# Kernel optimization log

Hardware: AMD Instinct MI355X
Metric: run time of the kernel (lower is better)

Reference implementation:

```python
import jax, jax.numpy as jnp
import numpy as np

D_MODEL = 1024
N_LAYER = 4
D_INNER = 2048   # expand * d_model
D_STATE = 16
D_CONV = 4
DT_RANK = 64     # ceil(d_model / 16)
B, L = 2, 1024
EPS = 1e-5


def setup_inputs() -> dict:
    key = jax.random.key(0)
    ks = jax.random.split(key, 10)
    nl = N_LAYER
    def nrm(k, shape, s=0.02):
        return jax.random.normal(k, shape, jnp.float32) * s
    A_log = jnp.broadcast_to(jnp.log(jnp.arange(1, D_STATE + 1, dtype=jnp.float32)),
                             (nl, D_INNER, D_STATE)) + jnp.zeros((nl, D_INNER, D_STATE), jnp.float32)
    return {
        "hidden_states": jax.random.normal(ks[0], (B, L, D_MODEL), jnp.float32),
        "in_proj_w": nrm(ks[1], (nl, 2 * D_INNER, D_MODEL)),
        "conv_w": nrm(ks[2], (nl, D_INNER, D_CONV), 0.1),
        "conv_b": nrm(ks[3], (nl, D_INNER), 0.02),
        "x_proj_w": nrm(ks[4], (nl, DT_RANK + 2 * D_STATE, D_INNER)),
        "dt_proj_w": nrm(ks[5], (nl, D_INNER, DT_RANK), DT_RANK ** -0.5),
        "dt_proj_b": jnp.log(jnp.expm1(jax.random.uniform(ks[6], (nl, D_INNER), jnp.float32, 1e-3, 0.1))),
        "A_log": A_log,
        "D": jnp.ones((nl, D_INNER), jnp.float32),
        "out_proj_w": nrm(ks[7], (nl, D_MODEL, D_INNER)),
        "norm_w": jnp.ones((nl, D_MODEL), jnp.float32),
        "norm_b": jnp.zeros((nl, D_MODEL), jnp.float32),
        "normf_w": jnp.ones((D_MODEL,), jnp.float32),
        "normf_b": jnp.zeros((D_MODEL,), jnp.float32),
    }


def _layernorm(x, w, b):
    mu = x.mean(-1, keepdims=True)
    var = ((x - mu) ** 2).mean(-1, keepdims=True)
    return (x - mu) * jax.lax.rsqrt(var + EPS) * w + b


def _mamba(h, iw, cw, cb, xw, dw, db, Alog, Dp, ow):
    Bn, Ln, _ = h.shape
    xz = jnp.einsum('bld,ed->ble', h, iw)          # [B,L,2*d_inner]
    x, z = jnp.split(xz, 2, axis=-1)
    # depthwise causal conv1d over time, kernel size D_CONV
    xp = jnp.pad(x, ((0, 0), (D_CONV - 1, 0), (0, 0)))
    xc = sum(xp[:, k:k + Ln, :] * cw[:, k] for k in range(D_CONV)) + cb
    x = jax.nn.silu(xc)
    dbl = jnp.einsum('bld,ed->ble', x, xw)         # [B,L,dt_rank+2*d_state]
    dt = dbl[..., :DT_RANK]
    Bm = dbl[..., DT_RANK:DT_RANK + D_STATE]
    Cm = dbl[..., DT_RANK + D_STATE:]
    dt = jax.nn.softplus(jnp.einsum('blr,dr->bld', dt, dw) + db)  # [B,L,d_inner]
    A = -jnp.exp(Alog)                              # [d_inner,d_state]

    def step(hc, inp):
        dt_t, B_t, C_t, x_t = inp                   # [B,d],[B,s],[B,s],[B,d]
        dA = jnp.exp(dt_t[:, :, None] * A)
        hc = hc * dA + (dt_t * x_t)[:, :, None] * B_t[:, None, :]
        y_t = jnp.einsum('bds,bs->bd', hc, C_t)
        return hc, y_t

    h0 = jnp.zeros((Bn, D_INNER, D_STATE), x.dtype)
    xs = (dt.transpose(1, 0, 2), Bm.transpose(1, 0, 2),
          Cm.transpose(1, 0, 2), x.transpose(1, 0, 2))
    _, ys = jax.lax.scan(step, h0, xs)              # ys: [L,B,d_inner]
    y = ys.transpose(1, 0, 2) + x * Dp
    y = y * jax.nn.silu(z)
    return jnp.einsum('bld,ed->ble', y, ow)


def reference(hidden_states, in_proj_w, conv_w, conv_b, x_proj_w, dt_proj_w,
              dt_proj_b, A_log, D, out_proj_w, norm_w, norm_b, normf_w, normf_b):
    hs = hidden_states
    residual = None
    for i in range(N_LAYER):
        residual = hs if residual is None else hs + residual
        hs = _layernorm(residual, norm_w[i], norm_b[i])
        hs = _mamba(hs, in_proj_w[i], conv_w[i], conv_b[i], x_proj_w[i],
                    dt_proj_w[i], dt_proj_b[i], A_log[i], D[i], out_proj_w[i])
    residual = hs + residual
    return _layernorm(residual, normf_w, normf_b)
```

## Files before the change

### kernel.cpp

```cpp
#include <hip/hip_runtime.h>
#include <math.h>

#define D_MODEL 1024
#define D_INNER 2048
#define D_STATE 16
#define D_CONV  4
#define DT_RANK 64
#define NB      2
#define LSEQ    1024
#define NROWS   (NB * LSEQ)
#define LN_EPS  1e-5f
#define N_LAYER 4
#define NCHUNK  32
#define TCH     (LSEQ / NCHUNK)

__device__ inline unsigned bfbits(float f) {
    unsigned u = __float_as_uint(f);
    return (u + 0x7fffu + ((u >> 16) & 1u)) >> 16;
}

__device__ inline float wave_sum(float s) {
    #pragma unroll
    for (int m = 1; m < 64; m <<= 1) s += __shfl_xor(s, m, 64);
    return s;
}

__global__ __launch_bounds__(256)
void add_ln_kernel(const float* __restrict__ add, float* __restrict__ residual,
                   const float* __restrict__ w, const float* __restrict__ b,
                   void* __restrict__ out, int first, int bf16out)
{
    int row = blockIdx.x;
    int tid = threadIdx.x;
    size_t base = (size_t)row * D_MODEL + tid * 4;

    float4 v = *(const float4*)(add + base);
    if (!first) {
        float4 r = *(const float4*)(residual + base);
        v.x += r.x; v.y += r.y; v.z += r.z; v.w += r.w;
    }
    *(float4*)(residual + base) = v;

    __shared__ float red[8];
    float s = v.x + v.y + v.z + v.w;
    s = wave_sum(s);
    if ((tid & 63) == 0) red[tid >> 6] = s;
    __syncthreads();
    float mu = (red[0] + red[1] + red[2] + red[3]) * (1.0f / D_MODEL);

    float dx = v.x - mu, dy = v.y - mu, dz = v.z - mu, dw2 = v.w - mu;
    float s2 = dx*dx + dy*dy + dz*dz + dw2*dw2;
    s2 = wave_sum(s2);
    if ((tid & 63) == 0) red[4 + (tid >> 6)] = s2;
    __syncthreads();
    float var = (red[4] + red[5] + red[6] + red[7]) * (1.0f / D_MODEL);
    float rs = rsqrtf(var + LN_EPS);

    float4 wv = *(const float4*)(w + tid * 4);
    float4 bv = *(const float4*)(b + tid * 4);
    float4 o;
    o.x = dx  * rs * wv.x + bv.x;
    o.y = dy  * rs * wv.y + bv.y;
    o.z = dz  * rs * wv.z + bv.z;
    o.w = dw2 * rs * wv.w + bv.w;
    if (bf16out) {
        ushort4 ov;
        ov.x = (unsigned short)bfbits(o.x);
        ov.y = (unsigned short)bfbits(o.y);
        ov.z = (unsigned short)bfbits(o.z);
        ov.w = (unsigned short)bfbits(o.w);
        *(ushort4*)((unsigned short*)out + base) = ov;
    } else {
        *(float4*)((float*)out + base) = o;
    }
}

__global__ __launch_bounds__(256)
void f32_to_bf16_kernel(const float* __restrict__ src, unsigned short* __restrict__ dst)
{
    int i = blockIdx.x * 256 + threadIdx.x;
    float4 v = *(const float4*)(src + (size_t)i * 4);
    ushort4 o;
    o.x = (unsigned short)bfbits(v.x);
    o.y = (unsigned short)bfbits(v.y);
    o.z = (unsigned short)bfbits(v.z);
    o.w = (unsigned short)bfbits(v.w);
    *(ushort4*)(dst + (size_t)i * 4) = o;
}

#define TILE 64
#define KT   16

__global__ __launch_bounds__(256)
void gemm_nt(const float* __restrict__ A, const float* __restrict__ B,
             float* __restrict__ C, int M, int N, int K,
             int lda, int ldb, int ldc,
             const float* __restrict__ bias, int mode)
{
    __shared__ float As[KT][TILE + 4];
    __shared__ float Bs[KT][TILE + 4];

    int tid = threadIdx.x;
    int tx = tid & 15, ty = tid >> 4;
    int m0 = blockIdx.y * TILE;
    int n0 = blockIdx.x * TILE;

    int lr = tid >> 2;
    int lk = (tid & 3) * 4;

    float acc[4][4] = {};

    for (int k0 = 0; k0 < K; k0 += KT) {
        {
            int m = m0 + lr;
            float4 v = *(const float4*)(A + (size_t)m * lda + k0 + lk);
            As[lk + 0][lr] = v.x; As[lk + 1][lr] = v.y;
            As[lk + 2][lr] = v.z; As[lk + 3][lr] = v.w;
        }
        {
            int n = n0 + lr;
            float4 v = make_float4(0.f, 0.f, 0.f, 0.f);
            if (n < N) v = *(const float4*)(B + (size_t)n * ldb + k0 + lk);
            Bs[lk + 0][lr] = v.x; Bs[lk + 1][lr] = v.y;
            Bs[lk + 2][lr] = v.z; Bs[lk + 3][lr] = v.w;
        }
        __syncthreads();
        #pragma unroll
        for (int kk = 0; kk < KT; ++kk) {
            float4 a4 = *(const float4*)&As[kk][ty * 4];
            float4 b4 = *(const float4*)&Bs[kk][tx * 4];
            float av[4] = {a4.x, a4.y, a4.z, a4.w};
            float bv[4] = {b4.x, b4.y, b4.z, b4.w};
            #pragma unroll
            for (int i = 0; i < 4; ++i)
                #pragma unroll
                for (int j = 0; j < 4; ++j)
                    acc[i][j] += av[i] * bv[j];
        }
        __syncthreads();
    }

    #pragma unroll
    for (int i = 0; i < 4; ++i) {
        int m = m0 + ty * 4 + i;
        #pragma unroll
        for (int j = 0; j < 4; ++j) {
            int n = n0 + tx * 4 + j;
            if (n >= N) continue;
            float v = acc[i][j];
            if (mode == 1) {
                v += bias[n];
                v = (v > 20.f) ? v : log1pf(__expf(v));
            }
            C[(size_t)m * ldc + n] = v;
        }
    }
}

__global__ __launch_bounds__(256)
void gemm_nt_splitk(const float* __restrict__ A, const float* __restrict__ B,
                    float* __restrict__ C, int M, int N, int K,
                    int lda, int ldb, int ldc, int kslice)
{
    __shared__ float As[KT][TILE + 4];
    __shared__ float Bs[KT][TILE + 4];

    int tid = threadIdx.x;
    int tx = tid & 15, ty = tid >> 4;
    int m0 = blockIdx.y * TILE;
    int n0 = blockIdx.x * TILE;
    int kb = blockIdx.z * kslice;

    int lr = tid >> 2;
    int lk = (tid & 3) * 4;

    float acc[4][4] = {};

    for (int k0 = kb; k0 < kb + kslice; k0 += KT) {
        {
            int m = m0 + lr;
            float4 v = *(const float4*)(A + (size_t)m * lda + k0 + lk);
            As[lk + 0][lr] = v.x; As[lk + 1][lr] = v.y;
            As[lk + 2][lr] = v.z; As[lk + 3][lr] = v.w;
        }
        {
            int n = n0 + lr;
            float4 v = make_float4(0.f, 0.f, 0.f, 0.f);
            if (n < N) v = *(const float4*)(B + (size_t)n * ldb + k0 + lk);
            Bs[lk + 0][lr] = v.x; Bs[lk + 1][lr] = v.y;
            Bs[lk + 2][lr] = v.z; Bs[lk + 3][lr] = v.w;
        }
        __syncthreads();
        #pragma unroll
        for (int kk = 0; kk < KT; ++kk) {
            float4 a4 = *(const float4*)&As[kk][ty * 4];
            float4 b4 = *(const float4*)&Bs[kk][tx * 4];
            float av[4] = {a4.x, a4.y, a4.z, a4.w};
            float bv[4] = {b4.x, b4.y, b4.z, b4.w};
            #pragma unroll
            for (int i = 0; i < 4; ++i)
                #pragma unroll
                for (int j = 0; j < 4; ++j)
                    acc[i][j] += av[i] * bv[j];
        }
        __syncthreads();
    }

    #pragma unroll
    for (int i = 0; i < 4; ++i) {
        int m = m0 + ty * 4 + i;
        #pragma unroll
        for (int j = 0; j < 4; ++j) {
            int n = n0 + tx * 4 + j;
            if (n < N) atomicAdd(&C[(size_t)m * ldc + n], acc[i][j]);
        }
    }
}

using bf16x8 = __attribute__((ext_vector_type(8))) short;
using f32x4  = __attribute__((ext_vector_type(4))) float;

#define BBM 128
#define BBN 128
#define BBK 64
#define LDS_S (BBK + 8)

__global__ __launch_bounds__(256)
void gemm_bf16_nt(const unsigned short* __restrict__ A, const unsigned short* __restrict__ Bw,
                  float* __restrict__ C, int M, int N, int K)
{
    __shared__ unsigned short As[BBM * LDS_S];
    __shared__ unsigned short Bs[BBN * LDS_S];

    int tid = threadIdx.x;
    int m0 = blockIdx.y * BBM, n0 = blockIdx.x * BBN;
    int lane = tid & 63, w = tid >> 6;
    int wm = (w >> 1) * 64, wn = (w & 1) * 64;
    int lm = lane & 15, q = lane >> 4;

    int lr = tid >> 3;
    int lc = (tid & 7) * 8;

    f32x4 acc[4][4] = {};

    for (int k0 = 0; k0 < K; k0 += BBK) {
        #pragma unroll
        for (int r = 0; r < 4; ++r) {
            int row = lr + r * 32;
            uint4 av = *(const uint4*)(A + (size_t)(m0 + row) * K + k0 + lc);
            *(uint4*)&As[row * LDS_S + lc] = av;
        }
        #pragma unroll
        for (int r = 0; r < 4; ++r) {
            int row = lr + r * 32;
            uint4 pv = *(const uint4*)(Bw + (size_t)(n0 + row) * K + k0 + lc);
            *(uint4*)&Bs[row * LDS_S + lc] = pv;
        }
        __syncthreads();
        #pragma unroll
        for (int kk = 0; kk < BBK; kk += 32) {
            bf16x8 af[4], bf[4];
            #pragma unroll
            for (int i = 0; i < 4; ++i)
                af[i] = *(const bf16x8*)&As[(wm + i * 16 + lm) * LDS_S + kk + q * 8];
            #pragma unroll
            for (int j = 0; j < 4; ++j)
                bf[j] = *(const bf16x8*)&Bs[(wn + j * 16 + lm) * LDS_S + kk + q * 8];
            #pragma unroll
            for (int i = 0; i < 4; ++i)
                #pragma unroll
                for (int j = 0; j < 4; ++j)
                    acc[i][j] = __builtin_amdgcn_mfma_f32_16x16x32_bf16(
                        af[i], bf[j], acc[i][j], 0, 0, 0);
        }
        __syncthreads();
    }

    #pragma unroll
    for (int i = 0; i < 4; ++i)
        #pragma unroll
        for (int j = 0; j < 4; ++j)
            #pragma unroll
            for (int r = 0; r < 4; ++r) {
                int row = m0 + wm + i * 16 + q * 4 + r;
                int col = n0 + wn + j * 16 + lm;
                C[(size_t)row * N + col] = acc[i][j][r];
            }
}

__global__ __launch_bounds__(256)
void conv_silu_kernel(const float* __restrict__ xz, const float* __restrict__ cw,
                      const float* __restrict__ cb, float* __restrict__ xc)
{
    int idx = blockIdx.x * 256 + threadIdx.x;
    int d  = idx & (D_INNER - 1);
    int t  = (idx >> 11) & (LSEQ - 1);
    int bb = idx >> 21;

    const float* xcol = xz + (size_t)bb * LSEQ * 2 * D_INNER + d;
    float acc = cb[d];
    #pragma unroll
    for (int k = 0; k < D_CONV; ++k) {
        int tt = t + k - (D_CONV - 1);
        if (tt >= 0) acc += xcol[(size_t)tt * 2 * D_INNER] * cw[d * D_CONV + k];
    }
    acc = acc / (1.f + __expf(-acc));
    xc[idx] = acc;
}

#define UNPK4(dst, off, v) { dst[(off)+0]=(v).x; dst[(off)+1]=(v).y; \
                             dst[(off)+2]=(v).z; dst[(off)+3]=(v).w; }

__global__ __launch_bounds__(256)
void scan_pass1(const float* __restrict__ dtb, const float* __restrict__ xc,
                const float* __restrict__ dbl, const float* __restrict__ Alog,
                float* __restrict__ aPbuf, float* __restrict__ bAbuf)
{
    int tid  = threadIdx.x;
    int half = tid & 1;
    int blk  = blockIdx.x;
    int dg   = blk & 15;
    int c    = (blk >> 4) & (NCHUNK - 1);
    int bb   = blk >> 9;
    int d    = dg * 128 + (tid >> 1);

    float A[8];
    {
        const float* pA = Alog + (size_t)d * D_STATE + half * 8;
        float4 v0 = *(const float4*)pA;
        float4 v1 = *(const float4*)(pA + 4);
        A[0] = -__expf(v0.x); A[1] = -__expf(v0.y);
        A[2] = -__expf(v0.z); A[3] = -__expf(v0.w);
        A[4] = -__expf(v1.x); A[5] = -__expf(v1.y);
        A[6] = -__expf(v1.z); A[7] = -__expf(v1.w);
    }

    size_t rowbase = (size_t)bb * LSEQ + (size_t)c * TCH;
    const float* pdt = dtb + rowbase * D_INNER + d;
    const float* pxc = xc  + rowbase * D_INNER + d;
    const float* pbc = dbl + rowbase * 96 + DT_RANK + half * 8;

    float aP[8] = {1.f,1.f,1.f,1.f,1.f,1.f,1.f,1.f};
    float bA[8] = {0.f,0.f,0.f,0.f,0.f,0.f,0.f,0.f};

    float  dtE = pdt[0], xvE = pxc[0];
    float4 BE0 = *(const float4*)pbc;
    float4 BE1 = *(const float4*)(pbc + 4);
    float  dtO = pdt[D_INNER], xvO = pxc[D_INNER];
    float4 BO0 = *(const float4*)(pbc + 96);
    float4 BO1 = *(const float4*)(pbc + 96 + 4);

    for (int t = 0; t < TCH; t += 2) {
        int t2 = (t + 2 < TCH) ? t + 2 : TCH - 1;
        int t3 = (t + 3 < TCH) ? t + 3 : TCH - 1;
        float  dtEn = pdt[(size_t)t2 * D_INNER], xvEn = pxc[(size_t)t2 * D_INNER];
        float4 BE0n = *(const float4*)(pbc + (size_t)t2 * 96);
        float4 BE1n = *(const float4*)(pbc + (size_t)t2 * 96 + 4);
        float  dtOn = pdt[(size_t)t3 * D_INNER], xvOn = pxc[(size_t)t3 * D_INNER];
        float4 BO0n = *(const float4*)(pbc + (size_t)t3 * 96);
        float4 BO1n = *(const float4*)(pbc + (size_t)t3 * 96 + 4);

        {
            float B[8];
            UNPK4(B, 0, BE0) UNPK4(B, 4, BE1)
            float dtx = dtE * xvE;
            #pragma unroll
            for (int s = 0; s < 8; ++s) {
                float a = __expf(dtE * A[s]);
                aP[s] *= a;
                bA[s] = bA[s] * a + dtx * B[s];
            }
        }
        {
            float B[8];
            UNPK4(B, 0, BO0) UNPK4(B, 4, BO1)
            float dtx = dtO * xvO;
            #pragma unroll
            for (int s = 0; s < 8; ++s) {
                float a = __expf(dtO * A[s]);
                aP[s] *= a;
                bA[s] = bA[s] * a + dtx * B[s];
            }
        }
        dtE = dtEn; xvE = xvEn; BE0 = BE0n; BE1 = BE1n;
        dtO = dtOn; xvO = xvOn; BO0 = BO0n; BO1 = BO1n;
    }

    float* pa = aPbuf + ((size_t)(bb * NCHUNK + c) * D_INNER + d) * D_STATE + half * 8;
    float* pb = bAbuf + ((size_t)(bb * NCHUNK + c) * D_INNER + d) * D_STATE + half * 8;
    *(float4*)(pa + 0) = make_float4(aP[0], aP[1], aP[2], aP[3]);
    *(float4*)(pa + 4) = make_float4(aP[4], aP[5], aP[6], aP[7]);
    *(float4*)(pb + 0) = make_float4(bA[0], bA[1], bA[2], bA[3]);
    *(float4*)(pb + 4) = make_float4(bA[4], bA[5], bA[6], bA[7]);
}

__global__ __launch_bounds__(256)
void scan_pass2(const float* __restrict__ dtb, const float* __restrict__ xc,
                const float* __restrict__ dbl, const float* __restrict__ xz,
                const float* __restrict__ Alog, const float* __restrict__ Dp,
                const float* __restrict__ aPbuf, const float* __restrict__ bAbuf,
                unsigned short* __restrict__ y)
{
    int tid  = threadIdx.x;
    int half = tid & 1;
    int blk  = blockIdx.x;
    int dg   = blk & 15;
    int c    = (blk >> 4) & (NCHUNK - 1);
    int bb   = blk >> 9;
    int d    = dg * 128 + (tid >> 1);

    float A[8];
    {
        const float* pA = Alog + (size_t)d * D_STATE + half * 8;
        float4 v0 = *(const float4*)pA;
        float4 v1 = *(const float4*)(pA + 4);
        A[0] = -__expf(v0.x); A[1] = -__expf(v0.y);
        A[2] = -__expf(v0.z); A[3] = -__expf(v0.w);
        A[4] = -__expf(v1.x); A[5] = -__expf(v1.y);
        A[6] = -__expf(v1.z); A[7] = -__expf(v1.w);
    }
    float Dd = Dp[d];

    float h[8] = {0.f,0.f,0.f,0.f,0.f,0.f,0.f,0.f};

    for (int cc = 0; cc < c; ++cc) {
        const float* pa = aPbuf + ((size_t)(bb * NCHUNK + cc) * D_INNER + d) * D_STATE + half * 8;
        const float* pb = bAbuf + ((size_t)(bb * NCHUNK + cc) * D_INNER + d) * D_STATE + half * 8;
        float4 a0 = *(const float4*)(pa + 0), a1 = *(const float4*)(pa + 4);
        float4 b0 = *(const float4*)(pb + 0), b1 = *(const float4*)(pb + 4);
        float av[8], bv[8];
        UNPK4(av, 0, a0) UNPK4(av, 4, a1)
        UNPK4(bv, 0, b0) UNPK4(bv, 4, b1)
        #pragma unroll
        for (int s = 0; s < 8; ++s) h[s] = h[s] * av[s] + bv[s];
    }

    size_t rowbase = (size_t)bb * LSEQ + (size_t)c * TCH;
    const float* pdt = dtb + rowbase * D_INNER + d;
    const float* pxc = xc  + rowbase * D_INNER + d;
    const float* pz  = xz  + rowbase * 2 * D_INNER + D_INNER + d;
    const float* pbc = dbl + rowbase * 96 + DT_RANK + half * 8;
    unsigned short* py = y + rowbase * D_INNER + d;

    float  dtE = pdt[0], xvE = pxc[0], zvE = pz[0];
    float4 BE0 = *(const float4*)pbc;
    float4 BE1 = *(const float4*)(pbc + 4);
    float4 CE0 = *(const float4*)(pbc + 16);
    float4 CE1 = *(const float4*)(pbc + 20);
    float  dtO = pdt[D_INNER], xvO = pxc[D_INNER], zvO = pz[2 * D_INNER];
    float4 BO0 = *(const float4*)(pbc + 96);
    float4 BO1 = *(const float4*)(pbc + 96 + 4);
    float4 CO0 = *(const float4*)(pbc + 96 + 16);
    float4 CO1 = *(const float4*)(pbc + 96 + 20);

    for (int t = 0; t < TCH; t += 2) {
        int t2 = (t + 2 < TCH) ? t + 2 : TCH - 1;
        int t3 = (t + 3 < TCH) ? t + 3 : TCH - 1;
        float  dtEn = pdt[(size_t)t2 * D_INNER], xvEn = pxc[(size_t)t2 * D_INNER];
        float  zvEn = pz[(size_t)t2 * 2 * D_INNER];
        float4 BE0n = *(const float4*)(pbc + (size_t)t2 * 96);
        float4 BE1n = *(const float4*)(pbc + (size_t)t2 * 96 + 4);
        float4 CE0n = *(const float4*)(pbc + (size_t)t2 * 96 + 16);
        float4 CE1n = *(const float4*)(pbc + (size_t)t2 * 96 + 20);
        float  dtOn = pdt[(size_t)t3 * D_INNER], xvOn = pxc[(size_t)t3 * D_INNER];
        float  zvOn = pz[(size_t)t3 * 2 * D_INNER];
        float4 BO0n = *(const float4*)(pbc + (size_t)t3 * 96);
        float4 BO1n = *(const float4*)(pbc + (size_t)t3 * 96 + 4);
        float4 CO0n = *(const float4*)(pbc + (size_t)t3 * 96 + 16);
        float4 CO1n = *(const float4*)(pbc + (size_t)t3 * 96 + 20);

        {
            float B[8], C[8];
            UNPK4(B, 0, BE0) UNPK4(B, 4, BE1)
            UNPK4(C, 0, CE0) UNPK4(C, 4, CE1)
            float dtx = dtE * xvE;
            float p = 0.f;
            #pragma unroll
            for (int s = 0; s < 8; ++s) {
                float a = __expf(dtE * A[s]);
                h[s] = h[s] * a + dtx * B[s];
                p += h[s] * C[s];
            }
            p += __shfl_xor(p, 1, 2);
            if (half == 0) {
                float sz = zvE / (1.f + __expf(-zvE));
                py[(size_t)t * D_INNER] = (unsigned short)bfbits((p + xvE * Dd) * sz);
            }
        }
        {
            float B[8], C[8];
            UNPK4(B, 0, BO0) UNPK4(B, 4, BO1)
            UNPK4(C, 0, CO0) UNPK4(C, 4, CO1)
            float dtx = dtO * xvO;
            float p = 0.f;
            #pragma unroll
            for (int s = 0; s < 8; ++s) {
                float a = __expf(dtO * A[s]);
                h[s] = h[s] * a + dtx * B[s];
                p += h[s] * C[s];
            }
            p += __shfl_xor(p, 1, 2);
            if (half == 0) {
                float sz = zvO / (1.f + __expf(-zvO));
                py[(size_t)(t + 1) * D_INNER] = (unsigned short)bfbits((p + xvO * Dd) * sz);
            }
        }
        dtE = dtEn; xvE = xvEn; zvE = zvEn;
        BE0 = BE0n; BE1 = BE1n; CE0 = CE0n; CE1 = CE1n;
        dtO = dtOn; xvO = xvOn; zvO = zvOn;
        BO0 = BO0n; BO1 = BO1n; CO0 = CO0n; CO1 = CO1n;
    }
}

extern "C" void kernel_launch(void* const* d_in, const int* in_sizes, int n_in,
                              void* d_out, int out_size, void* d_ws, size_t ws_size,
                              hipStream_t stream)
{
    const float* h_in  = (const float*)d_in[0];
    const float* iw    = (const float*)d_in[1];
    const float* cw    = (const float*)d_in[2];
    const float* cb    = (const float*)d_in[3];
    const float* xw    = (const float*)d_in[4];
    const float* dw    = (const float*)d_in[5];
    const float* db    = (const float*)d_in[6];
    const float* Alog  = (const float*)d_in[7];
    const float* Dp    = (const float*)d_in[8];
    const float* ow    = (const float*)d_in[9];
    const float* nw    = (const float*)d_in[10];
    const float* nb    = (const float*)d_in[11];
    const float* nfw   = (const float*)d_in[12];
    const float* nfb   = (const float*)d_in[13];

    float* ws = (float*)d_ws;
    float* residual = ws;
    float* hs       = residual + 2097152;
    float* xz       = hs + 2097152;
    float* xc       = xz + 8388608;
    float* dtb      = xc + 4194304;
    float* dbl      = dtb + 4194304;
    float* y        = dbl + 196608;

    float* aPbuf = hs;
    float* bAbuf = y + 2097152;

    unsigned short* wbuf_in  = (unsigned short*)y;
    unsigned short* hs_bf16  = (unsigned short*)(y + 2097152);
    unsigned short* y_bf16   = (unsigned short*)y;
    unsigned short* wbuf_out = (unsigned short*)dtb;

    const float* cur_add = h_in;
    for (int i = 0; i < N_LAYER; ++i) {
        add_ln_kernel<<<NROWS, 256, 0, stream>>>(cur_add, residual,
                                                 nw + i * D_MODEL, nb + i * D_MODEL,
                                                 hs_bf16, i == 0, 1);
        f32_to_bf16_kernel<<<(2 * D_INNER * D_MODEL) / 1024, 256, 0, stream>>>(
            iw + (size_t)i * 2 * D_INNER * D_MODEL, wbuf_in);
        gemm_bf16_nt<<<dim3(2 * D_INNER / BBN, NROWS / BBM), 256, 0, stream>>>(
            hs_bf16, wbuf_in, xz, NROWS, 2 * D_INNER, D_MODEL);
        conv_silu_kernel<<<NB * LSEQ * D_INNER / 256, 256, 0, stream>>>(
            xz, cw + (size_t)i * D_INNER * D_CONV, cb + i * D_INNER, xc);
        hipMemsetAsync(dbl, 0, 196608 * sizeof(float), stream);
        gemm_nt_splitk<<<dim3(2, NROWS / TILE, 8), 256, 0, stream>>>(
            xc, xw + (size_t)i * 96 * D_INNER, dbl,
            NROWS, 96, D_INNER, D_INNER, D_INNER, 96, D_INNER / 8);
        gemm_nt<<<dim3(D_INNER / TILE, NROWS / TILE), 256, 0, stream>>>(
            dbl, dw + (size_t)i * D_INNER * DT_RANK, dtb,
            NROWS, D_INNER, DT_RANK, 96, DT_RANK, D_INNER, db + i * D_INNER, 1);
        scan_pass1<<<NB * NCHUNK * (D_INNER / 128), 256, 0, stream>>>(
            dtb, xc, dbl, Alog + (size_t)i * D_INNER * D_STATE, aPbuf, bAbuf);
        scan_pass2<<<NB * NCHUNK * (D_INNER / 128), 256, 0, stream>>>(
            dtb, xc, dbl, xz, Alog + (size_t)i * D_INNER * D_STATE, Dp + i * D_INNER,
            aPbuf, bAbuf, y_bf16);
        f32_to_bf16_kernel<<<(D_MODEL * D_INNER) / 1024, 256, 0, stream>>>(
            ow + (size_t)i * D_MODEL * D_INNER, wbuf_out);
        gemm_bf16_nt<<<dim3(D_MODEL / BBN, NROWS / BBM), 256, 0, stream>>>(
            y_bf16, wbuf_out, hs, NROWS, D_MODEL, D_INNER);
        cur_add = hs;
    }
    add_ln_kernel<<<NROWS, 256, 0, stream>>>(hs, residual, nfw, nfb, d_out, 0, 0);
}
```

Baseline: 1.050 ms.

## Run x_proj and dt_proj GEMMs on MFMA using split bf16 hi/lo operands

Replaces the FP32 SIMT tiled GEMMs for x_proj (split-K with atomics) and dt_proj (with fused softplus) by MFMA kernels. Each operand is split into a bf16 high part and a bf16 low residual, and three MFMA products (hi*hi, hi*lo, lo*hi) approximate FP32 accuracy. The conv kernel now also emits the hi/lo copies of its output, and extra small kernels convert the weights and the dt-rank slice. This trades extra conversion passes and memory traffic for matrix-core throughput on two GEMMs that were running on scalar ALUs.

```diff
diff --git a/kernel.cpp b/kernel.cpp
--- a/kernel.cpp
+++ b/kernel.cpp
@@ -88,133 +88,37 @@
     *(ushort4*)(dst + (size_t)i * 4) = o;
 }
 
-#define TILE 64
-#define KT   16
-
-__global__ __launch_bounds__(256)
-void gemm_nt(const float* __restrict__ A, const float* __restrict__ B,
-             float* __restrict__ C, int M, int N, int K,
-             int lda, int ldb, int ldc,
-             const float* __restrict__ bias, int mode)
-{
-    __shared__ float As[KT][TILE + 4];
-    __shared__ float Bs[KT][TILE + 4];
-
-    int tid = threadIdx.x;
-    int tx = tid & 15, ty = tid >> 4;
-    int m0 = blockIdx.y * TILE;
-    int n0 = blockIdx.x * TILE;
-
-    int lr = tid >> 2;
-    int lk = (tid & 3) * 4;
-
-    float acc[4][4] = {};
-
-    for (int k0 = 0; k0 < K; k0 += KT) {
-        {
-            int m = m0 + lr;
-            float4 v = *(const float4*)(A + (size_t)m * lda + k0 + lk);
-            As[lk + 0][lr] = v.x; As[lk + 1][lr] = v.y;
-            As[lk + 2][lr] = v.z; As[lk + 3][lr] = v.w;
-        }
-        {
-            int n = n0 + lr;
-            float4 v = make_float4(0.f, 0.f, 0.f, 0.f);
-            if (n < N) v = *(const float4*)(B + (size_t)n * ldb + k0 + lk);
-            Bs[lk + 0][lr] = v.x; Bs[lk + 1][lr] = v.y;
-            Bs[lk + 2][lr] = v.z; Bs[lk + 3][lr] = v.w;
-        }
-        __syncthreads();
-        #pragma unroll
-        for (int kk = 0; kk < KT; ++kk) {
-            float4 a4 = *(const float4*)&As[kk][ty * 4];
-            float4 b4 = *(const float4*)&Bs[kk][tx * 4];
-            float av[4] = {a4.x, a4.y, a4.z, a4.w};
-            float bv[4] = {b4.x, b4.y, b4.z, b4.w};
-            #pragma unroll
-            for (int i = 0; i < 4; ++i)
-                #pragma unroll
-                for (int j = 0; j < 4; ++j)
-                    acc[i][j] += av[i] * bv[j];
-        }
-        __syncthreads();
-    }
-
-    #pragma unroll
-    for (int i = 0; i < 4; ++i) {
-        int m = m0 + ty * 4 + i;
-        #pragma unroll
-        for (int j = 0; j < 4; ++j) {
-            int n = n0 + tx * 4 + j;
-            if (n >= N) continue;
-            float v = acc[i][j];
-            if (mode == 1) {
-                v += bias[n];
-                v = (v > 20.f) ? v : log1pf(__expf(v));
-            }
-            C[(size_t)m * ldc + n] = v;
-        }
-    }
-}
-
-__global__ __launch_bounds__(256)
-void gemm_nt_splitk(const float* __restrict__ A, const float* __restrict__ B,
-                    float* __restrict__ C, int M, int N, int K,
-                    int lda, int ldb, int ldc, int kslice)
-{
-    __shared__ float As[KT][TILE + 4];
-    __shared__ float Bs[KT][TILE + 4];
-
-    int tid = threadIdx.x;
-    int tx = tid & 15, ty = tid >> 4;
-    int m0 = blockIdx.y * TILE;
-    int n0 = blockIdx.x * TILE;
-    int kb = blockIdx.z * kslice;
-
-    int lr = tid >> 2;
-    int lk = (tid & 3) * 4;
-
-    float acc[4][4] = {};
-
-    for (int k0 = kb; k0 < kb + kslice; k0 += KT) {
-        {
-            int m = m0 + lr;
-            float4 v = *(const float4*)(A + (size_t)m * lda + k0 + lk);
-            As[lk + 0][lr] = v.x; As[lk + 1][lr] = v.y;
-            As[lk + 2][lr] = v.z; As[lk + 3][lr] = v.w;
-        }
-        {
-            int n = n0 + lr;
-            float4 v = make_float4(0.f, 0.f, 0.f, 0.f);
-            if (n < N) v = *(const float4*)(B + (size_t)n * ldb + k0 + lk);
-            Bs[lk + 0][lr] = v.x; Bs[lk + 1][lr] = v.y;
-            Bs[lk + 2][lr] = v.z; Bs[lk + 3][lr] = v.w;
-        }
-        __syncthreads();
-        #pragma unroll
-        for (int kk = 0; kk < KT; ++kk) {
-            float4 a4 = *(const float4*)&As[kk][ty * 4];
-            float4 b4 = *(const float4*)&Bs[kk][tx * 4];
-            float av[4] = {a4.x, a4.y, a4.z, a4.w};
-            float bv[4] = {b4.x, b4.y, b4.z, b4.w};
-            #pragma unroll
-            for (int i = 0; i < 4; ++i)
-                #pragma unroll
-                for (int j = 0; j < 4; ++j)
-                    acc[i][j] += av[i] * bv[j];
-        }
-        __syncthreads();
-    }
-
-    #pragma unroll
-    for (int i = 0; i < 4; ++i) {
-        int m = m0 + ty * 4 + i;
-        #pragma unroll
-        for (int j = 0; j < 4; ++j) {
-            int n = n0 + tx * 4 + j;
-            if (n < N) atomicAdd(&C[(size_t)m * ldc + n], acc[i][j]);
-        }
-    }
+__global__ __launch_bounds__(256)
+void f32_to_hl_kernel(const float* __restrict__ src, unsigned short* __restrict__ hi,
+                      unsigned short* __restrict__ lo)
+{
+    int i = blockIdx.x * 256 + threadIdx.x;
+    float4 v = *(const float4*)(src + (size_t)i * 4);
+    ushort4 h, l;
+    float f;
+    h.x = (unsigned short)bfbits(v.x); f = __uint_as_float((unsigned)h.x << 16); l.x = (unsigned short)bfbits(v.x - f);
+    h.y = (unsigned short)bfbits(v.y); f = __uint_as_float((unsigned)h.y << 16); l.y = (unsigned short)bfbits(v.y - f);
+    h.z = (unsigned short)bfbits(v.z); f = __uint_as_float((unsigned)h.z << 16); l.z = (unsigned short)bfbits(v.z - f);
+    h.w = (unsigned short)bfbits(v.w); f = __uint_as_float((unsigned)h.w << 16); l.w = (unsigned short)bfbits(v.w - f);
+    *(ushort4*)(hi + (size_t)i * 4) = h;
+    *(ushort4*)(lo + (size_t)i * 4) = l;
+}
+
+__global__ __launch_bounds__(256)
+void dtlow_hl_kernel(const float* __restrict__ dbl, unsigned short* __restrict__ hi,
+                     unsigned short* __restrict__ lo)
+{
+    int idx = blockIdx.x * 256 + threadIdx.x;
+    int m = idx >> 4, k4 = (idx & 15) * 4;
+    float4 v = *(const float4*)(dbl + (size_t)m * 96 + k4);
+    ushort4 h, l;
+    float f;
+    h.x = (unsigned short)bfbits(v.x); f = __uint_as_float((unsigned)h.x << 16); l.x = (unsigned short)bfbits(v.x - f);
+    h.y = (unsigned short)bfbits(v.y); f = __uint_as_float((unsigned)h.y << 16); l.y = (unsigned short)bfbits(v.y - f);
+    h.z = (unsigned short)bfbits(v.z); f = __uint_as_float((unsigned)h.z << 16); l.z = (unsigned short)bfbits(v.z - f);
+    h.w = (unsigned short)bfbits(v.w); f = __uint_as_float((unsigned)h.w << 16); l.w = (unsigned short)bfbits(v.w - f);
+    *(ushort4*)(hi + (size_t)m * 64 + k4) = h;
+    *(ushort4*)(lo + (size_t)m * 64 + k4) = l;
 }
 
 using bf16x8 = __attribute__((ext_vector_type(8))) short;
@@ -289,8 +193,99 @@
 }
 
 __global__ __launch_bounds__(256)
+void xproj_hl(const unsigned short* __restrict__ Ah, const unsigned short* __restrict__ Al,
+              const unsigned short* __restrict__ Bh, const unsigned short* __restrict__ Bl,
+              float* __restrict__ C)
+{
+    int tid = threadIdx.x;
+    int lane = tid & 63, w = tid >> 6;
+    int lm = lane & 15, q = lane >> 4;
+    int m0 = blockIdx.x * 32;
+    int kb = blockIdx.y * 256;
+
+    int wm = (w & 1) * 16;
+    int wn = (w >> 1) * 48;
+
+    size_t arow = (size_t)(m0 + wm + lm) * 2048;
+
+    f32x4 acc[3] = {};
+
+    #pragma unroll 2
+    for (int kc = 0; kc < 8; ++kc) {
+        int k = kb + kc * 32 + q * 8;
+        bf16x8 ah = *(const bf16x8*)&Ah[arow + k];
+        bf16x8 al = *(const bf16x8*)&Al[arow + k];
+        #pragma unroll
+        for (int j = 0; j < 3; ++j) {
+            size_t brow = (size_t)(wn + j * 16 + lm) * 2048;
+            bf16x8 bh = *(const bf16x8*)&Bh[brow + k];
+            bf16x8 bl = *(const bf16x8*)&Bl[brow + k];
+            acc[j] = __builtin_amdgcn_mfma_f32_16x16x32_bf16(al, bh, acc[j], 0, 0, 0);
+            acc[j] = __builtin_amdgcn_mfma_f32_16x16x32_bf16(ah, bl, acc[j], 0, 0, 0);
+            acc[j] = __builtin_amdgcn_mfma_f32_16x16x32_bf16(ah, bh, acc[j], 0, 0, 0);
+        }
+    }
+
+    #pragma unroll
+    for (int j = 0; j < 3; ++j) {
+        int col = wn + j * 16 + lm;
+        #pragma unroll
+        for (int r = 0; r < 4; ++r) {
+            int row = m0 + wm + q * 4 + r;
+            atomicAdd(&C[(size_t)row * 96 + col], acc[j][r]);
+        }
+    }
+}
+
+__global__ __launch_bounds__(256)
+void dtproj_hl(const unsigned short* __restrict__ Ah, const unsigned short* __restrict__ Al,
+               const unsigned short* __restrict__ Bh, const unsigned short* __restrict__ Bl,
+               const float* __restrict__ bias, float* __restrict__ dtb)
+{
+    int tid = threadIdx.x;
+    int lane = tid & 63, w = tid >> 6;
+    int lm = lane & 15, q = lane >> 4;
+    int n0 = blockIdx.x * 128;
+    int m0 = blockIdx.y * 64;
+
+    size_t arow = (size_t)(m0 + w * 16 + lm) * 64;
+
+    f32x4 acc[8] = {};
+
+    #pragma unroll
+    for (int kc = 0; kc < 2; ++kc) {
+        int k = kc * 32 + q * 8;
+        bf16x8 ah = *(const bf16x8*)&Ah[arow + k];
+        bf16x8 al = *(const bf16x8*)&Al[arow + k];
+        #pragma unroll
+        for (int j = 0; j < 8; ++j) {
+            size_t brow = (size_t)(n0 + j * 16 + lm) * 64;
+            bf16x8 bh = *(const bf16x8*)&Bh[brow + k];
+            bf16x8 bl = *(const bf16x8*)&Bl[brow + k];
+            acc[j] = __builtin_amdgcn_mfma_f32_16x16x32_bf16(al, bh, acc[j], 0, 0, 0);
+            acc[j] = __builtin_amdgcn_mfma_f32_16x16x32_bf16(ah, bl, acc[j], 0, 0, 0);
+            acc[j] = __builtin_amdgcn_mfma_f32_16x16x32_bf16(ah, bh, acc[j], 0, 0, 0);
+        }
+    }
+
+    #pragma unroll
+    for (int j = 0; j < 8; ++j) {
+        int col = n0 + j * 16 + lm;
+        float bv = bias[col];
+        #pragma unroll
+        for (int r = 0; r < 4; ++r) {
+            int row = m0 + w * 16 + q * 4 + r;
+            float v = acc[j][r] + bv;
+            v = (v > 20.f) ? v : log1pf(__expf(v));
+            dtb[(size_t)row * D_INNER + col] = v;
+        }
+    }
+}
+
+__global__ __launch_bounds__(256)
 void conv_silu_kernel(const float* __restrict__ xz, const float* __restrict__ cw,
-                      const float* __restrict__ cb, float* __restrict__ xc)
+                      const float* __restrict__ cb, float* __restrict__ xc,
+                      unsigned short* __restrict__ xch, unsigned short* __restrict__ xcl)
 {
     int idx = blockIdx.x * 256 + threadIdx.x;
     int d  = idx & (D_INNER - 1);
@@ -306,6 +301,10 @@
     }
     acc = acc / (1.f + __expf(-acc));
     xc[idx] = acc;
+    unsigned hb = bfbits(acc);
+    xch[idx] = (unsigned short)hb;
+    float hf = __uint_as_float(hb << 16);
+    xcl[idx] = (unsigned short)bfbits(acc - hf);
 }
 
 #define UNPK4(dst, off, v) { dst[(off)+0]=(v).x; dst[(off)+1]=(v).y; \
@@ -546,6 +545,14 @@
     unsigned short* wbuf_in  = (unsigned short*)y;
     unsigned short* hs_bf16  = (unsigned short*)(y + 2097152);
     unsigned short* y_bf16   = (unsigned short*)y;
+    unsigned short* xc_hi    = (unsigned short*)y;
+    unsigned short* xc_lo    = (unsigned short*)(y + 2097152);
+    unsigned short* xwp_hi   = (unsigned short*)hs;
+    unsigned short* xwp_lo   = (unsigned short*)(hs + 98304);
+    unsigned short* dwp_hi   = (unsigned short*)(hs + 196608);
+    unsigned short* dwp_lo   = (unsigned short*)(hs + 262144);
+    unsigned short* dtl_hi   = (unsigned short*)(hs + 327680);
+    unsigned short* dtl_lo   = (unsigned short*)(hs + 393216);
     unsigned short* wbuf_out = (unsigned short*)dtb;
 
     const float* cur_add = h_in;
@@ -558,14 +565,17 @@
         gemm_bf16_nt<<<dim3(2 * D_INNER / BBN, NROWS / BBM), 256, 0, stream>>>(
             hs_bf16, wbuf_in, xz, NROWS, 2 * D_INNER, D_MODEL);
         conv_silu_kernel<<<NB * LSEQ * D_INNER / 256, 256, 0, stream>>>(
-            xz, cw + (size_t)i * D_INNER * D_CONV, cb + i * D_INNER, xc);
+            xz, cw + (size_t)i * D_INNER * D_CONV, cb + i * D_INNER, xc, xc_hi, xc_lo);
+        f32_to_hl_kernel<<<(96 * D_INNER) / 1024, 256, 0, stream>>>(
+            xw + (size_t)i * 96 * D_INNER, xwp_hi, xwp_lo);
+        f32_to_hl_kernel<<<(D_INNER * DT_RANK) / 1024, 256, 0, stream>>>(
+            dw + (size_t)i * D_INNER * DT_RANK, dwp_hi, dwp_lo);
         hipMemsetAsync(dbl, 0, 196608 * sizeof(float), stream);
-        gemm_nt_splitk<<<dim3(2, NROWS / TILE, 8), 256, 0, stream>>>(
-            xc, xw + (size_t)i * 96 * D_INNER, dbl,
-            NROWS, 96, D_INNER, D_INNER, D_INNER, 96, D_INNER / 8);
-        gemm_nt<<<dim3(D_INNER / TILE, NROWS / TILE), 256, 0, stream>>>(
-            dbl, dw + (size_t)i * D_INNER * DT_RANK, dtb,
-            NROWS, D_INNER, DT_RANK, 96, DT_RANK, D_INNER, db + i * D_INNER, 1);
+        xproj_hl<<<dim3(NROWS / 32, 8), 256, 0, stream>>>(
+            xc_hi, xc_lo, xwp_hi, xwp_lo, dbl);
+        dtlow_hl_kernel<<<(NROWS * 16) / 256, 256, 0, stream>>>(dbl, dtl_hi, dtl_lo);
+        dtproj_hl<<<dim3(D_INNER / 128, NROWS / 64), 256, 0, stream>>>(
+            dtl_hi, dtl_lo, dwp_hi, dwp_lo, db + i * D_INNER, dtb);
         scan_pass1<<<NB * NCHUNK * (D_INNER / 128), 256, 0, stream>>>(
             dtb, xc, dbl, Alog + (size_t)i * D_INNER * D_STATE, aPbuf, bAbuf);
         scan_pass2<<<NB * NCHUNK * (D_INNER / 128), 256, 0, stream>>>(
```

New measurement: 1.006 ms. 1.04x faster.
